# Kernel tuning notes

Measured on AMD Instinct MI355X. Metric: run time of the kernel, lower is better.

Reference implementation:

```python
import jax, jax.numpy as jnp
import numpy as np

N = 16                      # input_dim (state dimension)
EPS = 1e-6
TRIL_R, TRIL_C = np.tril_indices(N)   # 136 lower-triangular slots


def setup_inputs() -> dict:
    key = jax.random.key(0)
    ks = jax.random.split(key, 7)
    B = 131072
    def xavier(k, fan_in, fan_out):
        lim = float(np.sqrt(6.0 / (fan_in + fan_out)))
        return jax.random.uniform(k, (fan_in, fan_out), jnp.float32, -lim, lim)
    return {
        "points": jax.random.normal(ks[0], (B, N), jnp.float32),
        "W0": xavier(ks[1], N, 512),
        "b0": jax.random.normal(ks[2], (512,), jnp.float32) * 0.01,
        "W1": xavier(ks[3], 512, 512),
        "b1": jax.random.normal(ks[4], (512,), jnp.float32) * 0.01,
        "W2": xavier(ks[5], 512, 136),
        "b2": jax.random.normal(ks[6], (136,), jnp.float32) * 0.01,
    }


def reference(points, W0, b0, W1, b1, W2, b2):
    # MLP: tanh, tanh, identity
    h = jnp.tanh(points @ W0 + b0)
    h = jnp.tanh(h @ W1 + b1)
    net = h @ W2 + b2                         # [B, 136] tril entries
    B = points.shape[0]
    # Batched scatter into lower-triangular matrices M: [B, N, N]
    M = jnp.zeros((B, N, N), points.dtype).at[:, TRIL_R, TRIL_C].set(net)
    # x^T (M M^T) x == ||M^T x||^2
    y = jnp.einsum('bij,bi->bj', M, points)   # (M^T x)_j = sum_i M_ij x_i
    vals = jnp.sum(y * y, axis=-1) + EPS * jnp.sum(points * points, axis=-1)
    return vals.reshape(-1, 1)
```

## Files before the change

### kernel.cpp

```cpp
#include <hip/hip_runtime.h>

typedef __bf16 bf16x4 __attribute__((ext_vector_type(4)));
typedef __bf16 bf16x8 __attribute__((ext_vector_type(8)));
typedef float f32x16 __attribute__((ext_vector_type(16)));

#define W0F_OFF 0
#define W1F_OFF 8192
#define W2F_OFF (8192 + 262144)
#define PREP_TOTAL (8192 + 262144 + 81920)

__global__ void prep_weights(const float* __restrict__ W0,
                             const float* __restrict__ W1,
                             const float* __restrict__ W2,
                             __bf16* __restrict__ ws) {
    int t = blockIdx.x * 256 + threadIdx.x;
    if (t < 8192) {
        int j = t & 7, lane = (t >> 3) & 63, nt = t >> 9;
        int n = nt * 32 + (lane & 31);
        int k = (lane >> 5) * 8 + j;
        ws[W0F_OFF + t] = (__bf16)W0[k * 512 + n];
    } else if (t < 8192 + 262144) {
        int u = t - 8192;
        int j = u & 7, lane = (u >> 3) & 63;
        int x = u >> 9;
        int kk = x & 31, nt = x >> 5;
        int n = nt * 32 + (lane & 31);
        int k = kk * 16 + (lane >> 5) * 8 + j;
        ws[W1F_OFF + u] = (__bf16)W1[k * 512 + n];
    } else if (t < PREP_TOTAL) {
        int v = t - (8192 + 262144);
        int j = v & 7, lane = (v >> 3) & 63;
        int x = v >> 9;
        int kk = x & 31, nt = x >> 5;
        int n = nt * 32 + (lane & 31);
        int k = kk * 16 + (lane >> 5) * 8 + j;
        ws[W2F_OFF + v] = (n < 136) ? (__bf16)W2[k * 136 + n] : (__bf16)0.0f;
    }
}

__device__ __forceinline__ float fast_tanh(float x) {
#if __has_builtin(__builtin_amdgcn_exp2f)
    float e = __builtin_amdgcn_exp2f(x * 2.885390081777926f);
#else
    float e = exp2f(x * 2.885390081777926f);
#endif
    return 1.0f - 2.0f * __builtin_amdgcn_rcpf(e + 1.0f);
}

#define HSTR 520
#define NSTR 140

__global__ __launch_bounds__(512, 2)
void fused_mlp_quad(const float* __restrict__ points,
                    const float* __restrict__ b0,
                    const float* __restrict__ b1,
                    const float* __restrict__ b2,
                    const __bf16* __restrict__ ws,
                    float* __restrict__ out) {
    __shared__ __align__(16) unsigned char lds_raw[66560];
    __bf16* h  = (__bf16*)lds_raw;
    float* net = (float*)lds_raw;

    const __bf16* w0f = ws + W0F_OFF;
    const __bf16* w1f = ws + W1F_OFF;
    const __bf16* w2f = ws + W2F_OFF;

    const int tid = threadIdx.x;
    const int w   = tid >> 6;
    const int l   = tid & 63;
    const int ln  = l & 31;
    const int hi  = l >> 5;
    const int row0 = blockIdx.x * 64;

    const int lofs = l * 8;

    {
        bf16x8 bx[2];
#pragma unroll
        for (int bt = 0; bt < 2; ++bt) {
            const float* src = points + (row0 + bt * 32 + ln) * 16 + hi * 8;
            float4 p0 = ((const float4*)src)[0];
            float4 p1 = ((const float4*)src)[1];
            bf16x8 v;
            v[0] = (__bf16)p0.x; v[1] = (__bf16)p0.y; v[2] = (__bf16)p0.z; v[3] = (__bf16)p0.w;
            v[4] = (__bf16)p1.x; v[5] = (__bf16)p1.y; v[6] = (__bf16)p1.z; v[7] = (__bf16)p1.w;
            bx[bt] = v;
        }
#pragma unroll
        for (int t = 0; t < 2; ++t) {
            const int ntg = w * 2 + t;
            bf16x8 wf = *(const bf16x8*)(w0f + ntg * 512 + lofs);
#pragma unroll
            for (int bt = 0; bt < 2; ++bt) {
                f32x16 acc = {};
                acc = __builtin_amdgcn_mfma_f32_32x32x16_bf16(wf, bx[bt], acc, 0, 0, 0);
#pragma unroll
                for (int rg = 0; rg < 4; ++rg) {
                    const int n0 = ntg * 32 + 8 * rg + 4 * hi;
                    float4 bias = *(const float4*)(b0 + n0);
                    bf16x4 v;
                    v[0] = (__bf16)fast_tanh(acc[4 * rg + 0] + bias.x);
                    v[1] = (__bf16)fast_tanh(acc[4 * rg + 1] + bias.y);
                    v[2] = (__bf16)fast_tanh(acc[4 * rg + 2] + bias.z);
                    v[3] = (__bf16)fast_tanh(acc[4 * rg + 3] + bias.w);
                    *(bf16x4*)(h + (bt * 32 + ln) * HSTR + n0) = v;
                }
            }
        }
    }
    __syncthreads();

    f32x16 acc1[2][2] = {};
    {
        const __bf16* arow0 = h + ln * HSTR + hi * 8;
        const __bf16* arow1 = h + (32 + ln) * HSTR + hi * 8;
        const __bf16* wb0 = w1f + (w * 2 + 0) * 16384 + lofs;
        const __bf16* wb1 = w1f + (w * 2 + 1) * 16384 + lofs;
        for (int ks = 0; ks < 8; ++ks) {
            bf16x8 aa[4][2], bb[4][2];
#pragma unroll
            for (int u = 0; u < 4; ++u) {
                const int kk = ks * 4 + u;
                const int vo = kk * 512;
                aa[u][0] = *(const bf16x8*)(arow0 + kk * 16);
                aa[u][1] = *(const bf16x8*)(arow1 + kk * 16);
                bb[u][0] = *(const bf16x8*)(wb0 + vo);
                bb[u][1] = *(const bf16x8*)(wb1 + vo);
            }
#pragma unroll
            for (int u = 0; u < 4; ++u) {
#pragma unroll
                for (int t = 0; t < 2; ++t) {
                    acc1[0][t] = __builtin_amdgcn_mfma_f32_32x32x16_bf16(bb[u][t], aa[u][0], acc1[0][t], 0, 0, 0);
                    acc1[1][t] = __builtin_amdgcn_mfma_f32_32x32x16_bf16(bb[u][t], aa[u][1], acc1[1][t], 0, 0, 0);
                }
            }
        }
    }
    __syncthreads();
#pragma unroll
    for (int t = 0; t < 2; ++t) {
#pragma unroll
        for (int bt = 0; bt < 2; ++bt) {
#pragma unroll
            for (int rg = 0; rg < 4; ++rg) {
                const int n0 = (w * 2 + t) * 32 + 8 * rg + 4 * hi;
                float4 bias = *(const float4*)(b1 + n0);
                bf16x4 v;
                v[0] = (__bf16)fast_tanh(acc1[bt][t][4 * rg + 0] + bias.x);
                v[1] = (__bf16)fast_tanh(acc1[bt][t][4 * rg + 1] + bias.y);
                v[2] = (__bf16)fast_tanh(acc1[bt][t][4 * rg + 2] + bias.z);
                v[3] = (__bf16)fast_tanh(acc1[bt][t][4 * rg + 3] + bias.w);
                *(bf16x4*)(h + (bt * 32 + ln) * HSTR + n0) = v;
            }
        }
    }
    __syncthreads();

    f32x16 acc2a = {}, acc2e = {};
    const int nt2 = w >> 1;
    const int bt2 = w & 1;
    const bool two = (w < 2);
    {
        const __bf16* arowA = h + (bt2 * 32 + ln) * HSTR + hi * 8;
        const __bf16* arowE = h + ((w & 1) * 32 + ln) * HSTR + hi * 8;
        const __bf16* wbA = w2f + nt2 * 16384 + lofs;
        const __bf16* wbE = w2f + 4 * 16384 + lofs;
        for (int ks = 0; ks < 8; ++ks) {
            bf16x8 aaA[4], wA[4], aaE[4], wE[4];
#pragma unroll
            for (int u = 0; u < 4; ++u) {
                const int kk = ks * 4 + u;
                const int vo = kk * 512;
                aaA[u] = *(const bf16x8*)(arowA + kk * 16);
                wA[u]  = *(const bf16x8*)(wbA + vo);
                if (two) {
                    aaE[u] = *(const bf16x8*)(arowE + kk * 16);
                    wE[u]  = *(const bf16x8*)(wbE + vo);
                }
            }
#pragma unroll
            for (int u = 0; u < 4; ++u) {
                acc2a = __builtin_amdgcn_mfma_f32_32x32x16_bf16(wA[u], aaA[u], acc2a, 0, 0, 0);
                if (two)
                    acc2e = __builtin_amdgcn_mfma_f32_32x32x16_bf16(wE[u], aaE[u], acc2e, 0, 0, 0);
            }
        }
    }
    __syncthreads();
    {
#pragma unroll
        for (int rg = 0; rg < 4; ++rg) {
            const int n0 = nt2 * 32 + 8 * rg + 4 * hi;
            float4 bias = *(const float4*)(b2 + n0);
            float4 v;
            v.x = acc2a[4 * rg + 0] + bias.x;
            v.y = acc2a[4 * rg + 1] + bias.y;
            v.z = acc2a[4 * rg + 2] + bias.z;
            v.w = acc2a[4 * rg + 3] + bias.w;
            *(float4*)(net + (bt2 * 32 + ln) * NSTR + n0) = v;
        }
        if (two) {
            const int n0 = 128 + 4 * hi;
            float4 bias = *(const float4*)(b2 + n0);
            float4 v;
            v.x = acc2e[0] + bias.x;
            v.y = acc2e[1] + bias.y;
            v.z = acc2e[2] + bias.z;
            v.w = acc2e[3] + bias.w;
            *(float4*)(net + (w * 32 + ln) * NSTR + n0) = v;
        }
    }
    __syncthreads();

    {
        const int r  = tid >> 3;
        const int jg = tid & 7;
        const float* xp = points + (row0 + r) * 16;
        float xv[16];
#pragma unroll
        for (int i = 0; i < 4; ++i) {
            float4 v = ((const float4*)xp)[i];
            xv[i * 4 + 0] = v.x; xv[i * 4 + 1] = v.y;
            xv[i * 4 + 2] = v.z; xv[i * 4 + 3] = v.w;
        }
        float sumsq = 0.f;
#pragma unroll
        for (int i = 0; i < 16; ++i) sumsq += xv[i] * xv[i];
        float p = 0.f;
#pragma unroll
        for (int jj = 0; jj < 2; ++jj) {
            const int j = jg + jj * 8;
            float y = 0.f;
#pragma unroll
            for (int i = 0; i < 16; ++i) {
                float mv = net[r * NSTR + ((i * (i + 1)) >> 1) + j];
                y += (i >= j) ? mv * xv[i] : 0.f;
            }
            p += y * y;
        }
        p += __shfl_xor(p, 1);
        p += __shfl_xor(p, 2);
        p += __shfl_xor(p, 4);
        if (jg == 0) out[row0 + r] = p + 1e-6f * sumsq;
    }
}

extern "C" void kernel_launch(void* const* d_in, const int* in_sizes, int n_in,
                              void* d_out, int out_size, void* d_ws, size_t ws_size,
                              hipStream_t stream) {
    const float* points = (const float*)d_in[0];
    const float* W0 = (const float*)d_in[1];
    const float* b0 = (const float*)d_in[2];
    const float* W1 = (const float*)d_in[3];
    const float* b1 = (const float*)d_in[4];
    const float* W2 = (const float*)d_in[5];
    const float* b2 = (const float*)d_in[6];
    __bf16* ws = (__bf16*)d_ws;
    float* out = (float*)d_out;

    prep_weights<<<(PREP_TOTAL + 255) / 256, 256, 0, stream>>>(W0, W1, W2, ws);

    const int B = in_sizes[0] / 16;
    fused_mlp_quad<<<B / 64, 512, 0, stream>>>(points, b0, b1, b2, ws, out);
}
```

Baseline: 208.0 us.

## Double rows per block so each weight fragment feeds four batch tiles

Doubles the block to 1024 threads covering 128 rows. Each of the 16 waves now owns one 32-column output tile across four 32-row batch tiles, instead of two column tiles across two batch tiles. Each W1/W2 fragment loaded from global memory is reused by more MFMAs, which halves weight traffic per row and halves the number of blocks. The trade-off is 130KB of LDS per block, which likely limits each CU to one resident block, so barrier stalls are harder to hide behind other blocks.

Result: faster. 198.3 us (-4.7%).

```diff
diff --git a/kernel.cpp b/kernel.cpp
--- a/kernel.cpp
+++ b/kernel.cpp
@@ -50,14 +50,14 @@
 #define HSTR 520
 #define NSTR 140
 
-__global__ __launch_bounds__(512, 2)
+__global__ __launch_bounds__(1024, 4)
 void fused_mlp_quad(const float* __restrict__ points,
                     const float* __restrict__ b0,
                     const float* __restrict__ b1,
                     const float* __restrict__ b2,
                     const __bf16* __restrict__ ws,
                     float* __restrict__ out) {
-    __shared__ __align__(16) unsigned char lds_raw[66560];
+    __shared__ __align__(16) unsigned char lds_raw[133120];
     __bf16* h  = (__bf16*)lds_raw;
     float* net = (float*)lds_raw;
 
@@ -70,120 +70,105 @@
     const int l   = tid & 63;
     const int ln  = l & 31;
     const int hi  = l >> 5;
-    const int row0 = blockIdx.x * 64;
+    const int row0 = blockIdx.x * 128;
 
     const int lofs = l * 8;
 
     {
-        bf16x8 bx[2];
-#pragma unroll
-        for (int bt = 0; bt < 2; ++bt) {
+        bf16x8 wf = *(const bf16x8*)(w0f + w * 512 + lofs);
+#pragma unroll
+        for (int bt = 0; bt < 4; ++bt) {
             const float* src = points + (row0 + bt * 32 + ln) * 16 + hi * 8;
             float4 p0 = ((const float4*)src)[0];
             float4 p1 = ((const float4*)src)[1];
-            bf16x8 v;
-            v[0] = (__bf16)p0.x; v[1] = (__bf16)p0.y; v[2] = (__bf16)p0.z; v[3] = (__bf16)p0.w;
-            v[4] = (__bf16)p1.x; v[5] = (__bf16)p1.y; v[6] = (__bf16)p1.z; v[7] = (__bf16)p1.w;
-            bx[bt] = v;
-        }
-#pragma unroll
-        for (int t = 0; t < 2; ++t) {
-            const int ntg = w * 2 + t;
-            bf16x8 wf = *(const bf16x8*)(w0f + ntg * 512 + lofs);
-#pragma unroll
-            for (int bt = 0; bt < 2; ++bt) {
-                f32x16 acc = {};
-                acc = __builtin_amdgcn_mfma_f32_32x32x16_bf16(wf, bx[bt], acc, 0, 0, 0);
-#pragma unroll
-                for (int rg = 0; rg < 4; ++rg) {
-                    const int n0 = ntg * 32 + 8 * rg + 4 * hi;
-                    float4 bias = *(const float4*)(b0 + n0);
-                    bf16x4 v;
-                    v[0] = (__bf16)fast_tanh(acc[4 * rg + 0] + bias.x);
-                    v[1] = (__bf16)fast_tanh(acc[4 * rg + 1] + bias.y);
-                    v[2] = (__bf16)fast_tanh(acc[4 * rg + 2] + bias.z);
-                    v[3] = (__bf16)fast_tanh(acc[4 * rg + 3] + bias.w);
-                    *(bf16x4*)(h + (bt * 32 + ln) * HSTR + n0) = v;
-                }
-            }
-        }
-    }
-    __syncthreads();
-
-    f32x16 acc1[2][2] = {};
+            bf16x8 bx;
+            bx[0] = (__bf16)p0.x; bx[1] = (__bf16)p0.y; bx[2] = (__bf16)p0.z; bx[3] = (__bf16)p0.w;
+            bx[4] = (__bf16)p1.x; bx[5] = (__bf16)p1.y; bx[6] = (__bf16)p1.z; bx[7] = (__bf16)p1.w;
+            f32x16 acc = {};
+            acc = __builtin_amdgcn_mfma_f32_32x32x16_bf16(wf, bx, acc, 0, 0, 0);
+#pragma unroll
+            for (int rg = 0; rg < 4; ++rg) {
+                const int n0 = w * 32 + 8 * rg + 4 * hi;
+                float4 bias = *(const float4*)(b0 + n0);
+                bf16x4 v;
+                v[0] = (__bf16)fast_tanh(acc[4 * rg + 0] + bias.x);
+                v[1] = (__bf16)fast_tanh(acc[4 * rg + 1] + bias.y);
+                v[2] = (__bf16)fast_tanh(acc[4 * rg + 2] + bias.z);
+                v[3] = (__bf16)fast_tanh(acc[4 * rg + 3] + bias.w);
+                *(bf16x4*)(h + (bt * 32 + ln) * HSTR + n0) = v;
+            }
+        }
+    }
+    __syncthreads();
+
+    f32x16 acc1[4] = {};
     {
         const __bf16* arow0 = h + ln * HSTR + hi * 8;
         const __bf16* arow1 = h + (32 + ln) * HSTR + hi * 8;
-        const __bf16* wb0 = w1f + (w * 2 + 0) * 16384 + lofs;
-        const __bf16* wb1 = w1f + (w * 2 + 1) * 16384 + lofs;
+        const __bf16* arow2 = h + (64 + ln) * HSTR + hi * 8;
+        const __bf16* arow3 = h + (96 + ln) * HSTR + hi * 8;
+        const __bf16* wb = w1f + w * 16384 + lofs;
         for (int ks = 0; ks < 8; ++ks) {
-            bf16x8 aa[4][2], bb[4][2];
+            bf16x8 wf[4];
+#pragma unroll
+            for (int u = 0; u < 4; ++u)
+                wf[u] = *(const bf16x8*)(wb + (ks * 4 + u) * 512);
 #pragma unroll
             for (int u = 0; u < 4; ++u) {
-                const int kk = ks * 4 + u;
-                const int vo = kk * 512;
-                aa[u][0] = *(const bf16x8*)(arow0 + kk * 16);
-                aa[u][1] = *(const bf16x8*)(arow1 + kk * 16);
-                bb[u][0] = *(const bf16x8*)(wb0 + vo);
-                bb[u][1] = *(const bf16x8*)(wb1 + vo);
-            }
-#pragma unroll
-            for (int u = 0; u < 4; ++u) {
-#pragma unroll
-                for (int t = 0; t < 2; ++t) {
-                    acc1[0][t] = __builtin_amdgcn_mfma_f32_32x32x16_bf16(bb[u][t], aa[u][0], acc1[0][t], 0, 0, 0);
-                    acc1[1][t] = __builtin_amdgcn_mfma_f32_32x32x16_bf16(bb[u][t], aa[u][1], acc1[1][t], 0, 0, 0);
-                }
-            }
-        }
-    }
-    __syncthreads();
-#pragma unroll
-    for (int t = 0; t < 2; ++t) {
-#pragma unroll
-        for (int bt = 0; bt < 2; ++bt) {
-#pragma unroll
-            for (int rg = 0; rg < 4; ++rg) {
-                const int n0 = (w * 2 + t) * 32 + 8 * rg + 4 * hi;
-                float4 bias = *(const float4*)(b1 + n0);
-                bf16x4 v;
-                v[0] = (__bf16)fast_tanh(acc1[bt][t][4 * rg + 0] + bias.x);
-                v[1] = (__bf16)fast_tanh(acc1[bt][t][4 * rg + 1] + bias.y);
-                v[2] = (__bf16)fast_tanh(acc1[bt][t][4 * rg + 2] + bias.z);
-                v[3] = (__bf16)fast_tanh(acc1[bt][t][4 * rg + 3] + bias.w);
-                *(bf16x4*)(h + (bt * 32 + ln) * HSTR + n0) = v;
-            }
+                const int ko = (ks * 4 + u) * 16;
+                bf16x8 a0 = *(const bf16x8*)(arow0 + ko);
+                bf16x8 a1 = *(const bf16x8*)(arow1 + ko);
+                bf16x8 a2 = *(const bf16x8*)(arow2 + ko);
+                bf16x8 a3 = *(const bf16x8*)(arow3 + ko);
+                acc1[0] = __builtin_amdgcn_mfma_f32_32x32x16_bf16(wf[u], a0, acc1[0], 0, 0, 0);
+                acc1[1] = __builtin_amdgcn_mfma_f32_32x32x16_bf16(wf[u], a1, acc1[1], 0, 0, 0);
+                acc1[2] = __builtin_amdgcn_mfma_f32_32x32x16_bf16(wf[u], a2, acc1[2], 0, 0, 0);
+                acc1[3] = __builtin_amdgcn_mfma_f32_32x32x16_bf16(wf[u], a3, acc1[3], 0, 0, 0);
+            }
+        }
+    }
+    __syncthreads();
+#pragma unroll
+    for (int bt = 0; bt < 4; ++bt) {
+#pragma unroll
+        for (int rg = 0; rg < 4; ++rg) {
+            const int n0 = w * 32 + 8 * rg + 4 * hi;
+            float4 bias = *(const float4*)(b1 + n0);
+            bf16x4 v;
+            v[0] = (__bf16)fast_tanh(acc1[bt][4 * rg + 0] + bias.x);
+            v[1] = (__bf16)fast_tanh(acc1[bt][4 * rg + 1] + bias.y);
+            v[2] = (__bf16)fast_tanh(acc1[bt][4 * rg + 2] + bias.z);
+            v[3] = (__bf16)fast_tanh(acc1[bt][4 * rg + 3] + bias.w);
+            *(bf16x4*)(h + (bt * 32 + ln) * HSTR + n0) = v;
         }
     }
     __syncthreads();
 
     f32x16 acc2a = {}, acc2e = {};
-    const int nt2 = w >> 1;
-    const int bt2 = w & 1;
-    const bool two = (w < 2);
+    const int nt2 = w >> 2;
+    const int bt2 = w & 3;
+    const bool two = (w < 4);
     {
         const __bf16* arowA = h + (bt2 * 32 + ln) * HSTR + hi * 8;
-        const __bf16* arowE = h + ((w & 1) * 32 + ln) * HSTR + hi * 8;
+        const __bf16* arowE = h + ((w & 3) * 32 + ln) * HSTR + hi * 8;
         const __bf16* wbA = w2f + nt2 * 16384 + lofs;
         const __bf16* wbE = w2f + 4 * 16384 + lofs;
         for (int ks = 0; ks < 8; ++ks) {
-            bf16x8 aaA[4], wA[4], aaE[4], wE[4];
+            bf16x8 wA[4], wE[4];
 #pragma unroll
             for (int u = 0; u < 4; ++u) {
-                const int kk = ks * 4 + u;
-                const int vo = kk * 512;
-                aaA[u] = *(const bf16x8*)(arowA + kk * 16);
-                wA[u]  = *(const bf16x8*)(wbA + vo);
+                wA[u] = *(const bf16x8*)(wbA + (ks * 4 + u) * 512);
+                if (two) wE[u] = *(const bf16x8*)(wbE + (ks * 4 + u) * 512);
+            }
+#pragma unroll
+            for (int u = 0; u < 4; ++u) {
+                const int ko = (ks * 4 + u) * 16;
+                bf16x8 aA = *(const bf16x8*)(arowA + ko);
+                acc2a = __builtin_amdgcn_mfma_f32_32x32x16_bf16(wA[u], aA, acc2a, 0, 0, 0);
                 if (two) {
-                    aaE[u] = *(const bf16x8*)(arowE + kk * 16);
-                    wE[u]  = *(const bf16x8*)(wbE + vo);
+                    bf16x8 aE = *(const bf16x8*)(arowE + ko);
+                    acc2e = __builtin_amdgcn_mfma_f32_32x32x16_bf16(wE[u], aE, acc2e, 0, 0, 0);
                 }
-            }
-#pragma unroll
-            for (int u = 0; u < 4; ++u) {
-                acc2a = __builtin_amdgcn_mfma_f32_32x32x16_bf16(wA[u], aaA[u], acc2a, 0, 0, 0);
-                if (two)
-                    acc2e = __builtin_amdgcn_mfma_f32_32x32x16_bf16(wE[u], aaE[u], acc2e, 0, 0, 0);
             }
         }
     }
@@ -208,7 +193,7 @@
             v.y = acc2e[1] + bias.y;
             v.z = acc2e[2] + bias.z;
             v.w = acc2e[3] + bias.w;
-            *(float4*)(net + (w * 32 + ln) * NSTR + n0) = v;
+            *(float4*)(net + ((w & 3) * 32 + ln) * NSTR + n0) = v;
         }
     }
     __syncthreads();
@@ -262,5 +247,5 @@
     prep_weights<<<(PREP_TOTAL + 255) / 256, 256, 0, stream>>>(W0, W1, W2, ws);
 
     const int B = in_sizes[0] / 16;
-    fused_mlp_quad<<<B / 64, 512, 0, stream>>>(points, b0, b1, b2, ws, out);
-}
+    fused_mlp_quad<<<B / 128, 1024, 0, stream>>>(points, b0, b1, b2, ws, out);
+}
```
